# Kernel optimization log

Measured on AMD Instinct MI355X. Metric: run time of the kernel, lower is better.

The kernel has to match this reference:

```python
import jax, jax.numpy as jnp
import numpy as np

TEMP = 16.0  # sqrt(in_dim=256), module default when temperature=None
BN_EPS = 1e-5


def setup_inputs() -> dict:
    key = jax.random.key(0)
    ks = jax.random.split(key, 8)
    B, Cin, T, H, W = 8, 256, 8, 16, 16
    FF, Cout = 512, 256
    # small init scale keeps softmax logits in a sane range
    s = 0.02
    return {
        "x": jax.random.normal(ks[0], (B, Cin, T, H, W), jnp.float32),
        "Wk": jax.random.normal(ks[1], (FF, Cin), jnp.float32) * s,
        "Wq": jax.random.normal(ks[2], (FF, Cin), jnp.float32) * s,
        "Wv": jax.random.normal(ks[3], (FF, Cin), jnp.float32) * s,
        "Wout": jax.random.normal(ks[4], (Cout, FF), jnp.float32) * s,
        "bout": jax.random.normal(ks[5], (Cout,), jnp.float32) * s,
        "gamma": jnp.ones((Cout,), jnp.float32),
        "beta": jnp.zeros((Cout,), jnp.float32),
    }


def reference(x, Wk, Wq, Wv, Wout, bout, gamma, beta):
    B, Cin, T, H, W = x.shape
    N = T * H * W
    xf = x.reshape(B, Cin, N)                      # 1x1x1 conv == per-position matmul
    K = jnp.einsum('fc,bcn->bfn', Wk, xf)
    Q = jnp.einsum('fc,bcn->bfn', Wq, xf)
    V = jnp.einsum('fc,bcn->bfn', Wv, xf)
    KQ = jnp.einsum('bfi,bfj->bij', K, Q)          # [B, N, N] = K^T Q
    attn = jax.nn.softmax(KQ / TEMP, axis=2)
    # torch: sum(V[:, :, :, None] * attn[:, None], dim=3)
    #      = V[b,c,i] * sum_j attn[b,i,j]  (no need to materialize B x C x N x N)
    agg = V * jnp.sum(attn, axis=2)[:, None, :]    # [B, FF, N]
    o = jnp.einsum('of,bfn->bon', Wout, agg) + bout[None, :, None]
    o = jax.nn.relu(o).reshape(B, -1, T, H, W)
    y = x + o                                      # residual (in_dim == out_dim)
    # BatchNorm3d, training mode (fresh module): batch stats over (B, T, H, W)
    mean = jnp.mean(y, axis=(0, 2, 3, 4), keepdims=True)
    var = jnp.var(y, axis=(0, 2, 3, 4), keepdims=True)
    g = gamma[None, :, None, None, None]
    b = beta[None, :, None, None, None]
    return g * (y - mean) * jax.lax.rsqrt(var + BN_EPS) + b
```

## Files before the change

### kernel.cpp

```cpp
#include <hip/hip_runtime.h>

typedef __attribute__((ext_vector_type(8))) short short8;
typedef __attribute__((ext_vector_type(4))) float floatx4;
typedef __attribute__((ext_vector_type(4))) unsigned int uint32x4;

#define CIN  256
#define NSP  2048
#define COUT 256
#define FF   512
#define NSHARD 32
#define PITCH 128

__device__ unsigned short g_M[COUT * CIN];
__device__ float g_shard[NSHARD][2][COUT];

__device__ __forceinline__ unsigned short f2bf_rne(float f) {
  unsigned int u = __float_as_uint(f);
  u += 0x7fffu + ((u >> 16) & 1u);
  return (unsigned short)(u >> 16);
}

__device__ __forceinline__ unsigned int pack_bf16_hu(float lo, float hi) {
  unsigned int a = __float_as_uint(lo) + 0x8000u;
  unsigned int b = __float_as_uint(hi) + 0x8000u;
  return __builtin_amdgcn_perm(b, a, 0x07060302u);
}

__global__ __launch_bounds__(1024) void k1_m(
    const float* __restrict__ Wv, const float* __restrict__ Wout)
{
  __shared__ float ws[4 * FF];
  __shared__ float red[4][4][256];
  const int tid = threadIdx.x;
  const int r0  = blockIdx.x * 4;
  if (blockIdx.x == 0) {
    float* gs = &g_shard[0][0][0];
    #pragma unroll
    for (int i = 0; i < 16; ++i) gs[tid + i * 1024] = 0.f;
  }
  ws[tid]        = Wout[(size_t)r0 * FF + tid];
  ws[tid + 1024] = Wout[(size_t)r0 * FF + 1024 + tid];
  __syncthreads();
  const int c  = tid & 255;
  const int fs = tid >> 8;
  float a0 = 0.f, a1 = 0.f, a2 = 0.f, a3 = 0.f;
  #pragma unroll 8
  for (int f0 = 0; f0 < 128; ++f0) {
    const int f = fs * 128 + f0;
    const float wv = Wv[(size_t)f * 256 + c];
    a0 += ws[f] * wv;
    a1 += ws[FF + f] * wv;
    a2 += ws[2 * FF + f] * wv;
    a3 += ws[3 * FF + f] * wv;
  }
  red[fs][0][c] = a0; red[fs][1][c] = a1;
  red[fs][2][c] = a2; red[fs][3][c] = a3;
  __syncthreads();
  const int rr = tid >> 8, cc = tid & 255;
  float s = red[0][rr][cc] + red[1][rr][cc] + red[2][rr][cc] + red[3][rr][cc];
  g_M[(size_t)(r0 + rr) * 256 + cc] = f2bf_rne(s);
}

__global__ __launch_bounds__(512, 4) void k2_gemm(
    const float* __restrict__ x, const float* __restrict__ bout,
    float* __restrict__ out)
{
  __shared__ __align__(16) unsigned int lxt[64 * PITCH];
  __shared__ float ls[COUT], lq[COUT];
  const int tid  = threadIdx.x;
  const int lane = tid & 63;
  const int wave = tid >> 6;
  const int m16  = lane & 15;
  const int q    = lane >> 4;
  const int id   = blockIdx.x;
  const int b    = id & 7;
  const int n0   = (id >> 3) * 64;
  const int wocb = (wave & 3) * 64;
  const int wn   = (wave >> 2) * 32;

  if (tid < COUT) { ls[tid] = 0.f; lq[tid] = 0.f; }

  {
    const int cgrp = tid >> 4;
    const int n4   = tid & 15;
    const int c0   = cgrp * 8;
    const float* gp = x + (size_t)b * CIN * NSP + (size_t)c0 * NSP + n0 + n4 * 4;
    float4 v[8];
    #pragma unroll
    for (int i = 0; i < 8; ++i)
      v[i] = *(const float4*)(gp + (size_t)i * NSP);
    const float* vf = (const float*)v;
    #pragma unroll
    for (int j = 0; j < 4; ++j) {
      uint32x4 w;
      #pragma unroll
      for (int p = 0; p < 4; ++p)
        w[p] = pack_bf16_hu(vf[(2 * p) * 4 + j], vf[(2 * p + 1) * 4 + j]);
      const int n = n4 * 4 + j;
      const int idx = (n * PITCH + cgrp * 4) ^ ((n & 7) << 2);
      *(uint32x4*)&lxt[idx] = w;
    }
  }
  __syncthreads();

  floatx4 acc[4][2];
  #pragma unroll
  for (int i = 0; i < 4; ++i)
    #pragma unroll
    for (int j = 0; j < 2; ++j)
      acc[i][j] = (floatx4){0.f, 0.f, 0.f, 0.f};

  const unsigned short* Ab = g_M + (size_t)(wocb + m16) * 256 + q * 8;

  #pragma unroll
  for (int kk = 0; kk < 8; ++kk) {
    short8 av[4];
    #pragma unroll
    for (int ti = 0; ti < 4; ++ti)
      av[ti] = *(const short8*)(Ab + (size_t)ti * 16 * 256 + kk * 32);
    short8 bv[2];
    #pragma unroll
    for (int tj = 0; tj < 2; ++tj) {
      const int n = wn + tj * 16 + m16;
      const int idx = (n * PITCH + kk * 16 + q * 4) ^ ((n & 7) << 2);
      bv[tj] = *(const short8*)&lxt[idx];
    }
    #pragma unroll
    for (int ti = 0; ti < 4; ++ti)
      #pragma unroll
      for (int tj = 0; tj < 2; ++tj)
        acc[ti][tj] = __builtin_amdgcn_mfma_f32_16x16x32_bf16(av[ti], bv[tj], acc[ti][tj], 0, 0, 0);
  }

  #pragma unroll
  for (int ti = 0; ti < 4; ++ti) {
    #pragma unroll
    for (int r = 0; r < 4; ++r) {
      const int oc = wocb + ti * 16 + q * 4 + r;
      const float bo = bout[oc];
      float s = 0.f, s2 = 0.f;
      #pragma unroll
      for (int tj = 0; tj < 2; ++tj) {
        const int nl = wn + tj * 16 + m16;
        const size_t gidx = ((size_t)(b * COUT + oc)) * NSP + n0 + nl;
        float o = fmaxf(acc[ti][tj][r] + bo, 0.f);
        float y = x[gidx] + o;
        out[gidx] = y;
        s += y;
        s2 += y * y;
      }
      #pragma unroll
      for (int d = 1; d < 16; d <<= 1) {
        s  += __shfl_xor(s, d, 64);
        s2 += __shfl_xor(s2, d, 64);
      }
      if (m16 == 0) {
        atomicAdd(&ls[oc], s);
        atomicAdd(&lq[oc], s2);
      }
    }
  }
  __syncthreads();
  if (tid < COUT) {
    const int s = id >> 3;
    atomicAdd(&g_shard[s][0][tid], ls[tid]);
    atomicAdd(&g_shard[s][1][tid], lq[tid]);
  }
}

__global__ __launch_bounds__(256) void k3_norm(
    const float* __restrict__ gamma, const float* __restrict__ beta,
    float* __restrict__ out)
{
  const int id = blockIdx.x;
  const int b  = id & 7;
  const int oc = id >> 3;
  float su = 0.f, sq = 0.f;
  #pragma unroll
  for (int i = 0; i < NSHARD; ++i) {
    su += g_shard[i][0][oc];
    sq += g_shard[i][1][oc];
  }
  const float inv_n = 1.f / 16384.f;
  const float m  = su * inv_n;
  const float v  = sq * inv_n - m * m;
  const float sc = gamma[oc] * rsqrtf(v + 1e-5f);
  const float sh = beta[oc] - m * sc;
  float* p = out + ((size_t)(b * COUT + oc)) * NSP + threadIdx.x * 8;
  float4 a = *(const float4*)p;
  float4 c = *(const float4*)(p + 4);
  a.x = a.x * sc + sh; a.y = a.y * sc + sh;
  a.z = a.z * sc + sh; a.w = a.w * sc + sh;
  c.x = c.x * sc + sh; c.y = c.y * sc + sh;
  c.z = c.z * sc + sh; c.w = c.w * sc + sh;
  *(float4*)p = a;
  *(float4*)(p + 4) = c;
}

extern "C" void kernel_launch(void* const* d_in, const int* in_sizes, int n_in,
                              void* d_out, int out_size, void* d_ws, size_t ws_size,
                              hipStream_t stream) {
  const float* x     = (const float*)d_in[0];
  const float* Wv    = (const float*)d_in[3];
  const float* Wout  = (const float*)d_in[4];
  const float* bout  = (const float*)d_in[5];
  const float* gamma = (const float*)d_in[6];
  const float* beta  = (const float*)d_in[7];
  float* out = (float*)d_out;

  hipLaunchKernelGGL(k1_m,    dim3(64),   dim3(1024), 0, stream, Wv, Wout);
  hipLaunchKernelGGL(k2_gemm, dim3(256),  dim3(512),  0, stream, x, bout, out);
  hipLaunchKernelGGL(k3_norm, dim3(2048), dim3(256),  0, stream,
                     gamma, beta, out);
}
```

Baseline: 117.8 us.

## Fuse BatchNorm normalization into GEMM kernel via grid-wide spin barrier

```diff
diff --git a/kernel.cpp b/kernel.cpp
--- a/kernel.cpp
+++ b/kernel.cpp
@@ -13,6 +13,7 @@
 
 __device__ unsigned short g_M[COUT * CIN];
 __device__ float g_shard[NSHARD][2][COUT];
+__device__ unsigned int g_done;
 
 __device__ __forceinline__ unsigned short f2bf_rne(float f) {
   unsigned int u = __float_as_uint(f);
@@ -37,6 +38,7 @@
     float* gs = &g_shard[0][0][0];
     #pragma unroll
     for (int i = 0; i < 16; ++i) gs[tid + i * 1024] = 0.f;
+    if (tid == 0) g_done = 0u;
   }
   ws[tid]        = Wout[(size_t)r0 * FF + tid];
   ws[tid + 1024] = Wout[(size_t)r0 * FF + 1024 + tid];
@@ -63,6 +65,7 @@
 
 __global__ __launch_bounds__(512, 4) void k2_gemm(
     const float* __restrict__ x, const float* __restrict__ bout,
+    const float* __restrict__ gamma, const float* __restrict__ beta,
     float* __restrict__ out)
 {
   __shared__ __align__(16) unsigned int lxt[64 * PITCH];
@@ -145,7 +148,7 @@
         const size_t gidx = ((size_t)(b * COUT + oc)) * NSP + n0 + nl;
         float o = fmaxf(acc[ti][tj][r] + bo, 0.f);
         float y = x[gidx] + o;
-        out[gidx] = y;
+        acc[ti][tj][r] = y;
         s += y;
         s2 += y * y;
       }
@@ -165,36 +168,50 @@
     const int s = id >> 3;
     atomicAdd(&g_shard[s][0][tid], ls[tid]);
     atomicAdd(&g_shard[s][1][tid], lq[tid]);
-  }
-}
-
-__global__ __launch_bounds__(256) void k3_norm(
-    const float* __restrict__ gamma, const float* __restrict__ beta,
-    float* __restrict__ out)
-{
-  const int id = blockIdx.x;
-  const int b  = id & 7;
-  const int oc = id >> 3;
-  float su = 0.f, sq = 0.f;
-  #pragma unroll
-  for (int i = 0; i < NSHARD; ++i) {
-    su += g_shard[i][0][oc];
-    sq += g_shard[i][1][oc];
-  }
-  const float inv_n = 1.f / 16384.f;
-  const float m  = su * inv_n;
-  const float v  = sq * inv_n - m * m;
-  const float sc = gamma[oc] * rsqrtf(v + 1e-5f);
-  const float sh = beta[oc] - m * sc;
-  float* p = out + ((size_t)(b * COUT + oc)) * NSP + threadIdx.x * 8;
-  float4 a = *(const float4*)p;
-  float4 c = *(const float4*)(p + 4);
-  a.x = a.x * sc + sh; a.y = a.y * sc + sh;
-  a.z = a.z * sc + sh; a.w = a.w * sc + sh;
-  c.x = c.x * sc + sh; c.y = c.y * sc + sh;
-  c.z = c.z * sc + sh; c.w = c.w * sc + sh;
-  *(float4*)p = a;
-  *(float4*)(p + 4) = c;
+    __threadfence();
+  }
+  __syncthreads();
+
+  if (tid == 0) {
+    atomicAdd(&g_done, 1u);
+    while (__hip_atomic_load(&g_done, __ATOMIC_ACQUIRE,
+                             __HIP_MEMORY_SCOPE_AGENT) < gridDim.x)
+      __builtin_amdgcn_s_sleep(8);
+  }
+  __syncthreads();
+
+  if (tid < COUT) {
+    float su = 0.f, sq = 0.f;
+    #pragma unroll
+    for (int i = 0; i < NSHARD; ++i) {
+      su += __hip_atomic_load(&g_shard[i][0][tid], __ATOMIC_RELAXED,
+                              __HIP_MEMORY_SCOPE_AGENT);
+      sq += __hip_atomic_load(&g_shard[i][1][tid], __ATOMIC_RELAXED,
+                              __HIP_MEMORY_SCOPE_AGENT);
+    }
+    const float inv_n = 1.f / 16384.f;
+    const float m  = su * inv_n;
+    const float v  = sq * inv_n - m * m;
+    const float sc = gamma[tid] * rsqrtf(v + 1e-5f);
+    ls[tid] = sc;
+    lq[tid] = beta[tid] - m * sc;
+  }
+  __syncthreads();
+
+  #pragma unroll
+  for (int ti = 0; ti < 4; ++ti) {
+    #pragma unroll
+    for (int r = 0; r < 4; ++r) {
+      const int oc = wocb + ti * 16 + q * 4 + r;
+      const float sc = ls[oc], sh = lq[oc];
+      #pragma unroll
+      for (int tj = 0; tj < 2; ++tj) {
+        const int nl = wn + tj * 16 + m16;
+        const size_t gidx = ((size_t)(b * COUT + oc)) * NSP + n0 + nl;
+        out[gidx] = acc[ti][tj][r] * sc + sh;
+      }
+    }
+  }
 }
 
 extern "C" void kernel_launch(void* const* d_in, const int* in_sizes, int n_in,
@@ -208,8 +225,7 @@
   const float* beta  = (const float*)d_in[7];
   float* out = (float*)d_out;
 
-  hipLaunchKernelGGL(k1_m,    dim3(64),   dim3(1024), 0, stream, Wv, Wout);
-  hipLaunchKernelGGL(k2_gemm, dim3(256),  dim3(512),  0, stream, x, bout, out);
-  hipLaunchKernelGGL(k3_norm, dim3(2048), dim3(256),  0, stream,
-                     gamma, beta, out);
-}
+  hipLaunchKernelGGL(k1_m,    dim3(64),  dim3(1024), 0, stream, Wv, Wout);
+  hipLaunchKernelGGL(k2_gemm, dim3(256), dim3(512),  0, stream,
+                     x, bout, gamma, beta, out);
+}
```

After: 131.2 us. 1.11x slower.
